# Kernel optimization log

Hardware: AMD Instinct MI355X
Metric: run time of the kernel (lower is better)

The kernel has to match this reference:

```python
import jax, jax.numpy as jnp
import numpy as np

W_WIN = 5        # fine_window_size
D_F = 128        # fine d_model
D_C = 256        # coarse d_model
B, HF, WF = 2, 208, 208
WC = 104
LC = WC * WC
N = 5000


def setup_inputs() -> dict:
    key = jax.random.key(0)
    ks = jax.random.split(key, 12)
    inp = {
        'feat_f0': jax.random.normal(ks[0], (B, D_F, HF, WF), jnp.float32),
        'feat_f1': jax.random.normal(ks[1], (B, D_F, HF, WF), jnp.float32),
        'feat_c0': jax.random.normal(ks[2], (B, LC, D_C), jnp.float32),
        'feat_c1': jax.random.normal(ks[3], (B, LC, D_C), jnp.float32),
        # linear layer params (stored as [in, out]; torch weight is [out, in])
        'corr_fuse_w': jax.random.normal(ks[4], (3 * D_F, D_F), jnp.float32) * 0.05,
        'corr_fuse_b': jnp.zeros((D_F,), jnp.float32),
        'down_proj_w': jax.random.normal(ks[5], (D_C, D_F), jnp.float32) * 0.05,
        'down_proj_b': jnp.zeros((D_F,), jnp.float32),
        'merge_feat_w': jax.random.normal(ks[6], (2 * D_F, D_F), jnp.float32) * 0.05,
        'merge_feat_b': jnp.zeros((D_F,), jnp.float32),
        'b_ids': jax.random.randint(ks[7], (N,), 0, B),
        'i_ids': jax.random.randint(ks[8], (N,), 0, LC),
        'j_ids': jax.random.randint(ks[9], (N,), 0, LC),
        'w0c': WC,
        'w1c': WC,
    }
    return inp


def _extract_patches(feat, b_ids, x_ids, y_ids, W):
    # Equivalent to F.unfold(feat, W, stride=1, padding=W//2) followed by a
    # gather at linear index y*width+x: directly gather the WxW window
    # centered at (x, y) with zero padding. feat: [B, C, H, Wd].
    Bsz, C, H, Wd = feat.shape
    off = jnp.arange(W) - W // 2
    yy = (y_ids[:, None] + off)[:, :, None]          # [n, W, 1]
    xx = (x_ids[:, None] + off)[:, None, :]          # [n, 1, W]
    valid = (yy >= 0) & (yy < H) & (xx >= 0) & (xx < Wd)  # [n, W, W]
    yc = jnp.clip(yy, 0, H - 1)
    xc = jnp.clip(xx, 0, Wd - 1)
    # advanced-index gather -> [n, W, W, C] (kernel rows outer, cols inner,
    # channel last: matches unfold's C-major layout after view/transpose)
    p = feat[b_ids[:, None, None], :, yc, xc]
    p = p * valid[..., None].astype(feat.dtype)
    return p.reshape(p.shape[0], W * W, C)           # [n, ww, C]


def reference(feat_f0, feat_f1, feat_c0, feat_c1,
              corr_fuse_w, corr_fuse_b, down_proj_w, down_proj_b,
              merge_feat_w, merge_feat_b,
              b_ids, i_ids, j_ids, w0c, w1c):
    W = W_WIN
    ww = W * W
    d_f = feat_f0.shape[1]
    Hf0, Wf0 = feat_f0.shape[2], feat_f0.shape[3]
    Hf1, Wf1 = feat_f1.shape[2], feat_f1.shape[3]

    x0 = jnp.clip((i_ids % w0c) * 2, 0, Wf0 - 1)
    y0 = jnp.clip((i_ids // w0c) * 2, 0, Hf0 - 1)
    x1 = jnp.clip((j_ids % w1c) * 2, 0, Wf1 - 1)
    y1 = jnp.clip((j_ids // w1c) * 2, 0, Hf1 - 1)

    p0 = _extract_patches(feat_f0, b_ids, x0, y0, W)   # [N, ww, d_f]
    p1 = _extract_patches(feat_f1, b_ids, x1, y1, W)

    inv_s = 1.0 / (d_f ** 0.5)
    c_patch = p0 * p1 * inv_s
    ctx_map = feat_f1.mean(axis=(2, 3))[b_ids][:, None, :]   # [N, 1, d_f]
    c_uav = p0 * ctx_map * inv_s
    ctx_uav = feat_f0.mean(axis=(2, 3))[b_ids][:, None, :]
    c_map = p1 * ctx_uav * inv_s

    f0 = jnp.concatenate([c_patch, c_uav, c_map], -1) @ corr_fuse_w + corr_fuse_b
    f1 = jnp.concatenate([c_patch, c_map, c_uav], -1) @ corr_fuse_w + corr_fuse_b

    # cat_c_feat branch
    fc = jnp.concatenate([feat_c0[b_ids, i_ids], feat_c1[b_ids, j_ids]], 0)
    fc = fc @ down_proj_w + down_proj_b                       # [2N, d_f]
    fc_rep = jnp.broadcast_to(fc[:, None, :], (fc.shape[0], ww, fc.shape[1]))
    merged = jnp.concatenate([jnp.concatenate([f0, f1], 0), fc_rep], -1)
    merged = merged @ merge_feat_w + merge_feat_b             # [2N, ww, d_f]

    n = f0.shape[0]
    return merged[:n], merged[n:]
```

## Files before the change

kernel.cpp:

```cpp
#include <hip/hip_runtime.h>

#define HF   208
#define WF   208
#define D_C  256
#define LC   10816
#define NPTS 5000
#define HW   (HF*WF)
#define INV_S 0.08838834764831845f
#define PAD  136

typedef __bf16 bf16_t;
typedef __bf16 bf16x8 __attribute__((ext_vector_type(8)));
typedef float  f32x4  __attribute__((ext_vector_type(4)));

#define FTR_OFF   172032
#define FTR_BYTES ((size_t)2*2*HW*128*2)
#define G_OFF     (FTR_OFF + FTR_BYTES)
#define G_BYTES   ((size_t)2*NPTS*128*4)

__global__ __launch_bounds__(256) void transpose_kernel(
    const float* __restrict__ f0, const float* __restrict__ f1,
    bf16_t* __restrict__ ftr, float* __restrict__ ctxs) {
  __shared__ float tile[64][129];
  __shared__ float cred[128];
  int bid = blockIdx.x;
  int tb = bid / 676;
  int hw0 = (bid % 676) * 64;
  const float* src = (tb < 2 ? f0 : f1) + (size_t)((tb & 1) * 128) * HW;
  int tid = threadIdx.x;
  if (tid < 128) cred[tid] = 0.f;
  int w4 = (tid & 15) * 4, cr = tid >> 4;
  for (int c = cr; c < 128; c += 16) {
    f32x4 v = *(const f32x4*)&src[(size_t)c * HW + hw0 + w4];
#pragma unroll
    for (int j = 0; j < 4; ++j) tile[w4 + j][c] = v[j];
  }
  __syncthreads();
  bf16_t* dst = ftr + ((size_t)tb * HW + hw0) * 128;
  int cb = (tid & 15) * 8;
  float sums8[8] = {0, 0, 0, 0, 0, 0, 0, 0};
  for (int p = (tid >> 4); p < 64; p += 16) {
    bf16x8 v;
#pragma unroll
    for (int j = 0; j < 8; ++j) {
      float x = tile[p][cb + j];
      sums8[j] += x;
      v[j] = (bf16_t)x;
    }
    *(bf16x8*)(dst + (size_t)p * 128 + cb) = v;
  }
  int lane = tid & 63;
#pragma unroll
  for (int j = 0; j < 8; ++j) {
    float s = sums8[j];
    s += __shfl_down(s, 32, 64);
    s += __shfl_down(s, 16, 64);
    if (lane < 16) atomicAdd(&cred[cb + j], s);
  }
  __syncthreads();
  if (tid < 128) atomicAdd(&ctxs[tb * 128 + tid], cred[tid]);
}

__global__ __launch_bounds__(128) void prep_kernel(
    const float* __restrict__ corr_w, const float* __restrict__ corr_b,
    const float* __restrict__ dp_w,   const float* __restrict__ dp_b,
    const float* __restrict__ mg_w,   const float* __restrict__ mg_b,
    bf16_t* __restrict__ A_swz, bf16_t* __restrict__ Dm,
    float* __restrict__ bias_all) {
  int bid = blockIdx.x;
  int c = threadIdx.x;
  if (bid < 384) {
    int mat = bid >> 7, r = bid & 127;
    float acc = 0.f;
    for (int t = 0; t < 128; ++t)
      acc += corr_w[(mat * 128 + r) * 128 + t] * mg_w[t * 128 + c];
    if (mat == 0) acc *= INV_S;
    int ks = r >> 5, quad = (r & 31) >> 3, jj = r & 7;
    int nt = c >> 4, lr = c & 15;
    A_swz[mat * 16384 + (((nt * 4 + ks) * 64) + quad * 16 + lr) * 8 + jj] = (bf16_t)acc;
  } else if (bid < 640) {
    int r = bid - 384;
    float acc = 0.f;
    for (int t = 0; t < 128; ++t)
      acc += dp_w[r * 128 + t] * mg_w[(128 + t) * 128 + c];
    Dm[r * 128 + c] = (bf16_t)acc;
  } else {
    float acc = mg_b[c];
    for (int t = 0; t < 128; ++t) {
      acc += corr_b[t] * mg_w[t * 128 + c];
      acc += dp_b[t]   * mg_w[(128 + t) * 128 + c];
    }
    bias_all[c] = acc;
  }
}

__global__ __launch_bounds__(128) void g_kernel(
    const float* __restrict__ fc0, const float* __restrict__ fc1,
    const int* __restrict__ b_ids, const int* __restrict__ i_ids,
    const int* __restrict__ j_ids, const bf16_t* __restrict__ Dm,
    const float* __restrict__ bias_all, float* __restrict__ g) {
  __shared__ float s_src[16][D_C];
  int r0 = blockIdx.x * 16;
  int tid = threadIdx.x;
  for (int u = tid; u < 16 * D_C; u += 128) {
    int rr = u >> 8, t = u & 255;
    int r = r0 + rr;
    const float* src;
    int b, idx;
    if (r < NPTS) { b = b_ids[r]; idx = i_ids[r]; src = fc0; }
    else          { b = b_ids[r - NPTS]; idx = j_ids[r - NPTS]; src = fc1; }
    s_src[rr][t] = src[((size_t)b * LC + idx) * D_C + t];
  }
  __syncthreads();
  float acc[16];
#pragma unroll
  for (int rr = 0; rr < 16; ++rr) acc[rr] = 0.f;
  for (int t = 0; t < D_C; ++t) {
    float d = (float)Dm[t * 128 + tid];
#pragma unroll
    for (int rr = 0; rr < 16; ++rr) acc[rr] += s_src[rr][t] * d;
  }
  float bv = bias_all[tid];
#pragma unroll
  for (int rr = 0; rr < 16; ++rr) g[(size_t)(r0 + rr) * 128 + tid] = acc[rr] + bv;
}

__global__ __launch_bounds__(256, 6) void main_kernel(
    const bf16_t* __restrict__ ftr,
    const int* __restrict__ b_ids, const int* __restrict__ i_ids,
    const int* __restrict__ j_ids, const int* __restrict__ w0c_p,
    const int* __restrict__ w1c_p, const float* __restrict__ ctxs,
    const bf16_t* __restrict__ A_swz, const float* __restrict__ g,
    float* __restrict__ out) {
  __shared__ __align__(16) union {
    bf16_t sV[3][32][PAD];
    float  so[2][25][132];
  } sm;

  int n = blockIdx.x;
  int tid = threadIdx.x;
  int b = b_ids[n], ii = i_ids[n], jj = j_ids[n];
  int w0c = w0c_p[0], w1c = w1c_p[0];
  int x0 = min((ii % w0c) * 2, WF - 1), y0 = min((ii / w0c) * 2, HF - 1);
  int x1 = min((jj % w1c) * 2, WF - 1), y1 = min((jj / w1c) * 2, HF - 1);

  int grp = tid >> 3, e = tid & 7;
  if (grp < 25) {
    const bf16_t* base0 = ftr + (size_t)b * HW * 128;
    const bf16_t* base1 = ftr + (size_t)(2 + b) * HW * 128;
    int dy = grp / 5 - 2, dx = grp % 5 - 2;
    int ya = y0 + dy, xa = x0 + dx;
    int yb = y1 + dy, xb = x1 + dx;
    bool v0 = (ya >= 0 && ya < HF && xa >= 0 && xa < WF);
    bool v1 = (yb >= 0 && yb < HF && xb >= 0 && xb < WF);
    const bf16_t* r0 = base0 + ((size_t)(v0 ? ya * WF + xa : 0)) * 128;
    const bf16_t* r1 = base1 + ((size_t)(v1 ? yb * WF + xb : 0)) * 128;
    const float ksc = INV_S / (float)HW;
#pragma unroll
    for (int h = 0; h < 2; ++h) {
      int cb = h * 64 + e * 8;
      bf16x8 a0 = *(const bf16x8*)(r0 + cb);
      bf16x8 a1 = *(const bf16x8*)(r1 + cb);
      f32x4 cs0a = *(const f32x4*)&ctxs[b * 128 + cb];
      f32x4 cs0b = *(const f32x4*)&ctxs[b * 128 + cb + 4];
      f32x4 cs1a = *(const f32x4*)&ctxs[256 + b * 128 + cb];
      f32x4 cs1b = *(const f32x4*)&ctxs[256 + b * 128 + cb + 4];
      bf16x8 oP, o1, o2;
#pragma unroll
      for (int j = 0; j < 8; ++j) {
        float p0 = v0 ? (float)a0[j] : 0.f;
        float p1 = v1 ? (float)a1[j] : 0.f;
        float c0f = (j < 4 ? cs0a[j & 3] : cs0b[j & 3]) * ksc;
        float c1f = (j < 4 ? cs1a[j & 3] : cs1b[j & 3]) * ksc;
        oP[j] = (bf16_t)(p0 * p1);
        o1[j] = (bf16_t)(p0 * c1f);
        o2[j] = (bf16_t)(p1 * c0f);
      }
      *(bf16x8*)&sm.sV[0][grp][cb] = oP;
      *(bf16x8*)&sm.sV[1][grp][cb] = o1;
      *(bf16x8*)&sm.sV[2][grp][cb] = o2;
    }
  }
  __syncthreads();

  int w = tid >> 6, lane = tid & 63, quad = lane >> 4, lr = lane & 15;
  f32x4 accP[2][2] = {};
  f32x4 acc01[2][2] = {};
  f32x4 acc10[2][2] = {};

#pragma unroll
  for (int ks = 0; ks < 4; ++ks) {
    bf16x8 va[2][3];
#pragma unroll
    for (int mt = 0; mt < 2; ++mt)
#pragma unroll
      for (int m = 0; m < 3; ++m)
        va[mt][m] = *(const bf16x8*)&sm.sV[m][mt * 16 + lr][ks * 32 + quad * 8];
    bf16x8 vb[3][2];
#pragma unroll
    for (int m = 0; m < 3; ++m)
#pragma unroll
      for (int ntl = 0; ntl < 2; ++ntl) {
        int nt = w * 2 + ntl;
        vb[m][ntl] = *(const bf16x8*)(A_swz + m * 16384 + (((nt * 4 + ks) * 64) + lane) * 8);
      }
#pragma unroll
    for (int mt = 0; mt < 2; ++mt)
#pragma unroll
      for (int ntl = 0; ntl < 2; ++ntl) {
        accP[mt][ntl]  = __builtin_amdgcn_mfma_f32_16x16x32_bf16(va[mt][0], vb[0][ntl], accP[mt][ntl], 0, 0, 0);
        acc01[mt][ntl] = __builtin_amdgcn_mfma_f32_16x16x32_bf16(va[mt][1], vb[1][ntl], acc01[mt][ntl], 0, 0, 0);
        acc01[mt][ntl] = __builtin_amdgcn_mfma_f32_16x16x32_bf16(va[mt][2], vb[2][ntl], acc01[mt][ntl], 0, 0, 0);
        acc10[mt][ntl] = __builtin_amdgcn_mfma_f32_16x16x32_bf16(va[mt][2], vb[1][ntl], acc10[mt][ntl], 0, 0, 0);
        acc10[mt][ntl] = __builtin_amdgcn_mfma_f32_16x16x32_bf16(va[mt][1], vb[2][ntl], acc10[mt][ntl], 0, 0, 0);
      }
  }
  __syncthreads();

#pragma unroll
  for (int ntl = 0; ntl < 2; ++ntl) {
    int col = w * 32 + ntl * 16 + lr;
#pragma unroll
    for (int mt = 0; mt < 2; ++mt)
#pragma unroll
      for (int rg = 0; rg < 4; ++rg) {
        int row = mt * 16 + quad * 4 + rg;
        if (row < 25) {
          sm.so[0][row][col] = accP[mt][ntl][rg] + acc01[mt][ntl][rg];
          sm.so[1][row][col] = accP[mt][ntl][rg] + acc10[mt][ntl][rg];
        }
      }
  }
  __syncthreads();

  float* o0 = out + (size_t)n * 3200;
  float* o1 = out + (size_t)NPTS * 3200 + (size_t)n * 3200;
  const float* g0 = g + (size_t)n * 128;
  const float* g1 = g + (size_t)(NPTS + n) * 128;
  for (int i = tid; i < 800; i += 256) {
    int f = i * 4, r = f >> 7, c = f & 127;
    f32x4 gv0 = *(const f32x4*)(g0 + c);
    f32x4 gv1 = *(const f32x4*)(g1 + c);
    f32x4 v0 = *(const f32x4*)&sm.so[0][r][c];
    f32x4 v1 = *(const f32x4*)&sm.so[1][r][c];
    __builtin_nontemporal_store(v0 + gv0, (f32x4*)(o0 + f));
    __builtin_nontemporal_store(v1 + gv1, (f32x4*)(o1 + f));
  }
}

__global__ __launch_bounds__(256) void ctx_mean_f32_kernel(
    const float* __restrict__ f0, const float* __restrict__ f1,
    float* __restrict__ ctxs) {
  int id = blockIdx.x;
  const float* src = (id < 256 ? f0 : f1) + (size_t)(id & 255) * HW;
  float s = 0.f;
  for (int i = threadIdx.x; i < HW; i += 256) s += src[i];
  for (int off = 32; off > 0; off >>= 1) s += __shfl_down(s, off, 64);
  __shared__ float part[4];
  if ((threadIdx.x & 63) == 0) part[threadIdx.x >> 6] = s;
  __syncthreads();
  if (threadIdx.x == 0) ctxs[id] = part[0] + part[1] + part[2] + part[3];
}

__global__ __launch_bounds__(256, 4) void main_fallback_kernel(
    const float* __restrict__ f0, const float* __restrict__ f1,
    const float* __restrict__ fc0, const float* __restrict__ fc1,
    const int* __restrict__ b_ids, const int* __restrict__ i_ids,
    const int* __restrict__ j_ids, const int* __restrict__ w0c_p,
    const int* __restrict__ w1c_p, const float* __restrict__ ctxs,
    const float* __restrict__ bias_all, const bf16_t* __restrict__ A_swz,
    const bf16_t* __restrict__ Dm, float* __restrict__ out) {
  __shared__ __align__(16) bf16_t sV[3][32][PAD];
  __shared__ float sg[2][128];
  int n = blockIdx.x;
  int tid = threadIdx.x;
  int b = b_ids[n], ii = i_ids[n], jj = j_ids[n];
  int w0c = w0c_p[0], w1c = w1c_p[0];
  int x0 = min((ii % w0c) * 2, WF - 1), y0 = min((ii / w0c) * 2, HF - 1);
  int x1 = min((jj % w1c) * 2, WF - 1), y1 = min((jj / w1c) * 2, HF - 1);
  const float ksc = INV_S / (float)HW;
  int c = tid & 127, kh = tid >> 7;
  float cs0 = ctxs[b * 128 + c] * ksc;
  float cs1 = ctxs[256 + b * 128 + c] * ksc;
  const float* f0b = f0 + (size_t)(b * 128 + c) * HW;
  const float* f1b = f1 + (size_t)(b * 128 + c) * HW;
  for (int k = kh; k < 32; k += 2) {
    float p0 = 0.f, p1 = 0.f;
    if (k < 25) {
      int dy = k / 5 - 2, dx = k % 5 - 2;
      int ya = y0 + dy, xa = x0 + dx;
      if (ya >= 0 && ya < HF && xa >= 0 && xa < WF) p0 = f0b[ya * WF + xa];
      int yb = y1 + dy, xb = x1 + dx;
      if (yb >= 0 && yb < HF && xb >= 0 && xb < WF) p1 = f1b[yb * WF + xb];
    }
    sV[0][k][c] = (bf16_t)(p0 * p1);
    sV[1][k][c] = (bf16_t)(p0 * cs1);
    sV[2][k][c] = (bf16_t)(p1 * cs0);
  }
  {
    int h = tid >> 7, col = tid & 127;
    const float* fcrow = h ? fc1 + ((size_t)b * LC + jj) * D_C
                           : fc0 + ((size_t)b * LC + ii) * D_C;
    float acc = 0.f;
#pragma unroll 8
    for (int t = 0; t < D_C; ++t) acc += fcrow[t] * (float)Dm[t * 128 + col];
    sg[h][col] = acc;
  }
  __syncthreads();
  int w = tid >> 6, lane = tid & 63, quad = lane >> 4, lr = lane & 15;
  f32x4 accP[2][2] = {}, acc01[2][2] = {}, acc10[2][2] = {};
#pragma unroll
  for (int ks = 0; ks < 4; ++ks) {
    bf16x8 va[2][3];
#pragma unroll
    for (int mt = 0; mt < 2; ++mt)
#pragma unroll
      for (int m = 0; m < 3; ++m)
        va[mt][m] = *(const bf16x8*)&sV[m][mt * 16 + lr][ks * 32 + quad * 8];
    bf16x8 vb[3][2];
#pragma unroll
    for (int m = 0; m < 3; ++m)
#pragma unroll
      for (int ntl = 0; ntl < 2; ++ntl) {
        int nt = w * 2 + ntl;
        vb[m][ntl] = *(const bf16x8*)(A_swz + m * 16384 + (((nt * 4 + ks) * 64) + lane) * 8);
      }
#pragma unroll
    for (int mt = 0; mt < 2; ++mt)
#pragma unroll
      for (int ntl = 0; ntl < 2; ++ntl) {
        accP[mt][ntl]  = __builtin_amdgcn_mfma_f32_16x16x32_bf16(va[mt][0], vb[0][ntl], accP[mt][ntl], 0, 0, 0);
        acc01[mt][ntl] = __builtin_amdgcn_mfma_f32_16x16x32_bf16(va[mt][1], vb[1][ntl], acc01[mt][ntl], 0, 0, 0);
        acc01[mt][ntl] = __builtin_amdgcn_mfma_f32_16x16x32_bf16(va[mt][2], vb[2][ntl], acc01[mt][ntl], 0, 0, 0);
        acc10[mt][ntl] = __builtin_amdgcn_mfma_f32_16x16x32_bf16(va[mt][2], vb[1][ntl], acc10[mt][ntl], 0, 0, 0);
        acc10[mt][ntl] = __builtin_amdgcn_mfma_f32_16x16x32_bf16(va[mt][1], vb[2][ntl], acc10[mt][ntl], 0, 0, 0);
      }
  }
#pragma unroll
  for (int ntl = 0; ntl < 2; ++ntl) {
    int col = w * 32 + ntl * 16 + lr;
    float bg = bias_all[col];
    float gg0 = sg[0][col] + bg, gg1 = sg[1][col] + bg;
#pragma unroll
    for (int mt = 0; mt < 2; ++mt)
#pragma unroll
      for (int rg = 0; rg < 4; ++rg) {
        int row = mt * 16 + quad * 4 + rg;
        if (row < 25) {
          size_t o = ((size_t)n * 25 + row) * 128 + col;
          out[o] = accP[mt][ntl][rg] + acc01[mt][ntl][rg] + gg0;
          out[(size_t)NPTS * 25 * 128 + o] = accP[mt][ntl][rg] + acc10[mt][ntl][rg] + gg1;
        }
      }
  }
}

extern "C" void kernel_launch(void* const* d_in, const int* in_sizes, int n_in,
                              void* d_out, int out_size, void* d_ws, size_t ws_size,
                              hipStream_t stream) {
  const float* f0     = (const float*)d_in[0];
  const float* f1     = (const float*)d_in[1];
  const float* fc0    = (const float*)d_in[2];
  const float* fc1    = (const float*)d_in[3];
  const float* corr_w = (const float*)d_in[4];
  const float* corr_b = (const float*)d_in[5];
  const float* dp_w   = (const float*)d_in[6];
  const float* dp_b   = (const float*)d_in[7];
  const float* mg_w   = (const float*)d_in[8];
  const float* mg_b   = (const float*)d_in[9];
  const int* b_ids    = (const int*)d_in[10];
  const int* i_ids    = (const int*)d_in[11];
  const int* j_ids    = (const int*)d_in[12];
  const int* w0c      = (const int*)d_in[13];
  const int* w1c      = (const int*)d_in[14];

  char* ws = (char*)d_ws;
  float*  ctxs     = (float*)(ws);
  float*  bias_all = (float*)(ws + 4096);
  bf16_t* A_swz    = (bf16_t*)(ws + 8192);
  bf16_t* Dm       = (bf16_t*)(ws + 106496);
  bf16_t* ftr      = (bf16_t*)(ws + FTR_OFF);
  float*  g        = (float*)(ws + G_OFF);
  int fast = (ws_size >= G_OFF + G_BYTES) ? 1 : 0;

  prep_kernel<<<641, 128, 0, stream>>>(corr_w, corr_b, dp_w, dp_b, mg_w, mg_b,
                                       A_swz, Dm, bias_all);
  if (fast) {
    hipMemsetAsync(ctxs, 0, 2048, stream);
    transpose_kernel<<<2704, 256, 0, stream>>>(f0, f1, ftr, ctxs);
    g_kernel<<<625, 128, 0, stream>>>(fc0, fc1, b_ids, i_ids, j_ids, Dm,
                                      bias_all, g);
    main_kernel<<<NPTS, 256, 0, stream>>>(ftr, b_ids, i_ids, j_ids, w0c, w1c,
                                          ctxs, A_swz, g, (float*)d_out);
  } else {
    ctx_mean_f32_kernel<<<512, 256, 0, stream>>>(f0, f1, ctxs);
    main_fallback_kernel<<<NPTS, 256, 0, stream>>>(f0, f1, fc0, fc1, b_ids,
                                                   i_ids, j_ids, w0c, w1c, ctxs,
                                                   bias_all, A_swz, Dm,
                                                   (float*)d_out);
  }
}
```

Baseline: 361.4 us.

## Fuse weight prep into transpose kernel and compute coarse projection inside main kernel

```diff
diff --git a/kernel.cpp b/kernel.cpp
--- a/kernel.cpp
+++ b/kernel.cpp
@@ -15,19 +15,53 @@
 
 #define FTR_OFF   172032
 #define FTR_BYTES ((size_t)2*2*HW*128*2)
-#define G_OFF     (FTR_OFF + FTR_BYTES)
-#define G_BYTES   ((size_t)2*NPTS*128*4)
-
-__global__ __launch_bounds__(256) void transpose_kernel(
+
+__global__ __launch_bounds__(256) void prep_transpose_kernel(
     const float* __restrict__ f0, const float* __restrict__ f1,
+    const float* __restrict__ corr_w, const float* __restrict__ corr_b,
+    const float* __restrict__ dp_w,   const float* __restrict__ dp_b,
+    const float* __restrict__ mg_w,   const float* __restrict__ mg_b,
+    bf16_t* __restrict__ A_swz, bf16_t* __restrict__ DmT,
+    float* __restrict__ bias_all,
     bf16_t* __restrict__ ftr, float* __restrict__ ctxs) {
   __shared__ float tile[64][129];
   __shared__ float cred[128];
   int bid = blockIdx.x;
+  int tid = threadIdx.x;
+
+  if (bid < 641) {
+    if (tid >= 128) return;
+    int c = tid;
+    if (bid < 384) {
+      int mat = bid >> 7, r = bid & 127;
+      float acc = 0.f;
+      for (int t = 0; t < 128; ++t)
+        acc += corr_w[(mat * 128 + r) * 128 + t] * mg_w[t * 128 + c];
+      if (mat == 0) acc *= INV_S;
+      int ks = r >> 5, quad = (r & 31) >> 3, jj = r & 7;
+      int nt = c >> 4, lr = c & 15;
+      A_swz[mat * 16384 + (((nt * 4 + ks) * 64) + quad * 16 + lr) * 8 + jj] = (bf16_t)acc;
+    } else if (bid < 640) {
+      int r = bid - 384;
+      float acc = 0.f;
+      for (int t = 0; t < 128; ++t)
+        acc += dp_w[r * 128 + t] * mg_w[(128 + t) * 128 + c];
+      DmT[c * 256 + r] = (bf16_t)acc;
+    } else {
+      float acc = mg_b[c];
+      for (int t = 0; t < 128; ++t) {
+        acc += corr_b[t] * mg_w[t * 128 + c];
+        acc += dp_b[t]   * mg_w[(128 + t) * 128 + c];
+      }
+      bias_all[c] = acc;
+    }
+    return;
+  }
+
+  bid -= 641;
   int tb = bid / 676;
   int hw0 = (bid % 676) * 64;
   const float* src = (tb < 2 ? f0 : f1) + (size_t)((tb & 1) * 128) * HW;
-  int tid = threadIdx.x;
   if (tid < 128) cred[tid] = 0.f;
   int w4 = (tid & 15) * 4, cr = tid >> 4;
   for (int c = cr; c < 128; c += 16) {
@@ -61,81 +95,19 @@
   if (tid < 128) atomicAdd(&ctxs[tb * 128 + tid], cred[tid]);
 }
 
-__global__ __launch_bounds__(128) void prep_kernel(
-    const float* __restrict__ corr_w, const float* __restrict__ corr_b,
-    const float* __restrict__ dp_w,   const float* __restrict__ dp_b,
-    const float* __restrict__ mg_w,   const float* __restrict__ mg_b,
-    bf16_t* __restrict__ A_swz, bf16_t* __restrict__ Dm,
-    float* __restrict__ bias_all) {
-  int bid = blockIdx.x;
-  int c = threadIdx.x;
-  if (bid < 384) {
-    int mat = bid >> 7, r = bid & 127;
-    float acc = 0.f;
-    for (int t = 0; t < 128; ++t)
-      acc += corr_w[(mat * 128 + r) * 128 + t] * mg_w[t * 128 + c];
-    if (mat == 0) acc *= INV_S;
-    int ks = r >> 5, quad = (r & 31) >> 3, jj = r & 7;
-    int nt = c >> 4, lr = c & 15;
-    A_swz[mat * 16384 + (((nt * 4 + ks) * 64) + quad * 16 + lr) * 8 + jj] = (bf16_t)acc;
-  } else if (bid < 640) {
-    int r = bid - 384;
-    float acc = 0.f;
-    for (int t = 0; t < 128; ++t)
-      acc += dp_w[r * 128 + t] * mg_w[(128 + t) * 128 + c];
-    Dm[r * 128 + c] = (bf16_t)acc;
-  } else {
-    float acc = mg_b[c];
-    for (int t = 0; t < 128; ++t) {
-      acc += corr_b[t] * mg_w[t * 128 + c];
-      acc += dp_b[t]   * mg_w[(128 + t) * 128 + c];
-    }
-    bias_all[c] = acc;
-  }
-}
-
-__global__ __launch_bounds__(128) void g_kernel(
-    const float* __restrict__ fc0, const float* __restrict__ fc1,
-    const int* __restrict__ b_ids, const int* __restrict__ i_ids,
-    const int* __restrict__ j_ids, const bf16_t* __restrict__ Dm,
-    const float* __restrict__ bias_all, float* __restrict__ g) {
-  __shared__ float s_src[16][D_C];
-  int r0 = blockIdx.x * 16;
-  int tid = threadIdx.x;
-  for (int u = tid; u < 16 * D_C; u += 128) {
-    int rr = u >> 8, t = u & 255;
-    int r = r0 + rr;
-    const float* src;
-    int b, idx;
-    if (r < NPTS) { b = b_ids[r]; idx = i_ids[r]; src = fc0; }
-    else          { b = b_ids[r - NPTS]; idx = j_ids[r - NPTS]; src = fc1; }
-    s_src[rr][t] = src[((size_t)b * LC + idx) * D_C + t];
-  }
-  __syncthreads();
-  float acc[16];
-#pragma unroll
-  for (int rr = 0; rr < 16; ++rr) acc[rr] = 0.f;
-  for (int t = 0; t < D_C; ++t) {
-    float d = (float)Dm[t * 128 + tid];
-#pragma unroll
-    for (int rr = 0; rr < 16; ++rr) acc[rr] += s_src[rr][t] * d;
-  }
-  float bv = bias_all[tid];
-#pragma unroll
-  for (int rr = 0; rr < 16; ++rr) g[(size_t)(r0 + rr) * 128 + tid] = acc[rr] + bv;
-}
-
 __global__ __launch_bounds__(256, 6) void main_kernel(
     const bf16_t* __restrict__ ftr,
+    const float* __restrict__ fc0, const float* __restrict__ fc1,
     const int* __restrict__ b_ids, const int* __restrict__ i_ids,
     const int* __restrict__ j_ids, const int* __restrict__ w0c_p,
     const int* __restrict__ w1c_p, const float* __restrict__ ctxs,
-    const bf16_t* __restrict__ A_swz, const float* __restrict__ g,
-    float* __restrict__ out) {
+    const bf16_t* __restrict__ A_swz, const bf16_t* __restrict__ DmT,
+    const float* __restrict__ bias_all, float* __restrict__ out) {
   __shared__ __align__(16) union {
     bf16_t sV[3][32][PAD];
-    float  so[2][25][132];
+    float  so[2][25 * 128];
   } sm;
+  __shared__ __align__(16) float sg[2][128];
 
   int n = blockIdx.x;
   int tid = threadIdx.x;
@@ -181,6 +153,25 @@
       *(bf16x8*)&sm.sV[2][grp][cb] = o2;
     }
   }
+
+  {
+    int h = tid >> 7, col = tid & 127;
+    const float* fcrow = h ? fc1 + ((size_t)b * LC + jj) * D_C
+                           : fc0 + ((size_t)b * LC + ii) * D_C;
+    const bf16_t* dcol = DmT + col * 256;
+    float p0 = 0.f, p1 = 0.f, p2 = 0.f, p3 = 0.f;
+#pragma unroll 4
+    for (int t = 0; t < D_C; t += 8) {
+      bf16x8 d  = *(const bf16x8*)(dcol + t);
+      f32x4  fa = *(const f32x4*)(fcrow + t);
+      f32x4  fb = *(const f32x4*)(fcrow + t + 4);
+      p0 += fa[0] * (float)d[0] + fb[0] * (float)d[4];
+      p1 += fa[1] * (float)d[1] + fb[1] * (float)d[5];
+      p2 += fa[2] * (float)d[2] + fb[2] * (float)d[6];
+      p3 += fa[3] * (float)d[3] + fb[3] * (float)d[7];
+    }
+    sg[h][col] = bias_all[col] + ((p0 + p1) + (p2 + p3));
+  }
   __syncthreads();
 
   int w = tid >> 6, lane = tid & 63, quad = lane >> 4, lr = lane & 15;
@@ -226,8 +217,8 @@
       for (int rg = 0; rg < 4; ++rg) {
         int row = mt * 16 + quad * 4 + rg;
         if (row < 25) {
-          sm.so[0][row][col] = accP[mt][ntl][rg] + acc01[mt][ntl][rg];
-          sm.so[1][row][col] = accP[mt][ntl][rg] + acc10[mt][ntl][rg];
+          sm.so[0][row * 128 + col] = accP[mt][ntl][rg] + acc01[mt][ntl][rg];
+          sm.so[1][row * 128 + col] = accP[mt][ntl][rg] + acc10[mt][ntl][rg];
         }
       }
   }
@@ -235,14 +226,12 @@
 
   float* o0 = out + (size_t)n * 3200;
   float* o1 = out + (size_t)NPTS * 3200 + (size_t)n * 3200;
-  const float* g0 = g + (size_t)n * 128;
-  const float* g1 = g + (size_t)(NPTS + n) * 128;
   for (int i = tid; i < 800; i += 256) {
-    int f = i * 4, r = f >> 7, c = f & 127;
-    f32x4 gv0 = *(const f32x4*)(g0 + c);
-    f32x4 gv1 = *(const f32x4*)(g1 + c);
-    f32x4 v0 = *(const f32x4*)&sm.so[0][r][c];
-    f32x4 v1 = *(const f32x4*)&sm.so[1][r][c];
+    int f = i * 4, c = f & 127;
+    f32x4 gv0 = *(const f32x4*)&sg[0][c];
+    f32x4 gv1 = *(const f32x4*)&sg[1][c];
+    f32x4 v0 = *(const f32x4*)&sm.so[0][f];
+    f32x4 v1 = *(const f32x4*)&sm.so[1][f];
     __builtin_nontemporal_store(v0 + gv0, (f32x4*)(o0 + f));
     __builtin_nontemporal_store(v1 + gv1, (f32x4*)(o1 + f));
   }
@@ -269,7 +258,7 @@
     const int* __restrict__ j_ids, const int* __restrict__ w0c_p,
     const int* __restrict__ w1c_p, const float* __restrict__ ctxs,
     const float* __restrict__ bias_all, const bf16_t* __restrict__ A_swz,
-    const bf16_t* __restrict__ Dm, float* __restrict__ out) {
+    const bf16_t* __restrict__ DmT, float* __restrict__ out) {
   __shared__ __align__(16) bf16_t sV[3][32][PAD];
   __shared__ float sg[2][128];
   int n = blockIdx.x;
@@ -301,10 +290,19 @@
     int h = tid >> 7, col = tid & 127;
     const float* fcrow = h ? fc1 + ((size_t)b * LC + jj) * D_C
                            : fc0 + ((size_t)b * LC + ii) * D_C;
-    float acc = 0.f;
-#pragma unroll 8
-    for (int t = 0; t < D_C; ++t) acc += fcrow[t] * (float)Dm[t * 128 + col];
-    sg[h][col] = acc;
+    const bf16_t* dcol = DmT + col * 256;
+    float p0 = 0.f, p1 = 0.f, p2 = 0.f, p3 = 0.f;
+#pragma unroll 4
+    for (int t = 0; t < D_C; t += 8) {
+      bf16x8 d  = *(const bf16x8*)(dcol + t);
+      f32x4  fa = *(const f32x4*)(fcrow + t);
+      f32x4  fb = *(const f32x4*)(fcrow + t + 4);
+      p0 += fa[0] * (float)d[0] + fb[0] * (float)d[4];
+      p1 += fa[1] * (float)d[1] + fb[1] * (float)d[5];
+      p2 += fa[2] * (float)d[2] + fb[2] * (float)d[6];
+      p3 += fa[3] * (float)d[3] + fb[3] * (float)d[7];
+    }
+    sg[h][col] = ((p0 + p1) + (p2 + p3));
   }
   __syncthreads();
   int w = tid >> 6, lane = tid & 63, quad = lane >> 4, lr = lane & 15;
@@ -378,25 +376,26 @@
   float*  ctxs     = (float*)(ws);
   float*  bias_all = (float*)(ws + 4096);
   bf16_t* A_swz    = (bf16_t*)(ws + 8192);
-  bf16_t* Dm       = (bf16_t*)(ws + 106496);
+  bf16_t* DmT      = (bf16_t*)(ws + 106496);
   bf16_t* ftr      = (bf16_t*)(ws + FTR_OFF);
-  float*  g        = (float*)(ws + G_OFF);
-  int fast = (ws_size >= G_OFF + G_BYTES) ? 1 : 0;
-
-  prep_kernel<<<641, 128, 0, stream>>>(corr_w, corr_b, dp_w, dp_b, mg_w, mg_b,
-                                       A_swz, Dm, bias_all);
+  int fast = (ws_size >= FTR_OFF + FTR_BYTES) ? 1 : 0;
+
   if (fast) {
     hipMemsetAsync(ctxs, 0, 2048, stream);
-    transpose_kernel<<<2704, 256, 0, stream>>>(f0, f1, ftr, ctxs);
-    g_kernel<<<625, 128, 0, stream>>>(fc0, fc1, b_ids, i_ids, j_ids, Dm,
-                                      bias_all, g);
-    main_kernel<<<NPTS, 256, 0, stream>>>(ftr, b_ids, i_ids, j_ids, w0c, w1c,
-                                          ctxs, A_swz, g, (float*)d_out);
+    prep_transpose_kernel<<<3345, 256, 0, stream>>>(
+        f0, f1, corr_w, corr_b, dp_w, dp_b, mg_w, mg_b,
+        A_swz, DmT, bias_all, ftr, ctxs);
+    main_kernel<<<NPTS, 256, 0, stream>>>(ftr, fc0, fc1, b_ids, i_ids, j_ids,
+                                          w0c, w1c, ctxs, A_swz, DmT, bias_all,
+                                          (float*)d_out);
   } else {
+    prep_transpose_kernel<<<641, 256, 0, stream>>>(
+        f0, f1, corr_w, corr_b, dp_w, dp_b, mg_w, mg_b,
+        A_swz, DmT, bias_all, ftr, ctxs);
     ctx_mean_f32_kernel<<<512, 256, 0, stream>>>(f0, f1, ctxs);
     main_fallback_kernel<<<NPTS, 256, 0, stream>>>(f0, f1, fc0, fc1, b_ids,
                                                    i_ids, j_ids, w0c, w1c, ctxs,
-                                                   bias_all, A_swz, Dm,
+                                                   bias_all, A_swz, DmT,
                                                    (float*)d_out);
   }
 }
```

Result: slower. 411.6 us (+13.9%).
